# Kernel tuning notes

Measured on AMD Instinct MI355X. Metric: run time of the kernel, lower is better.

Reference implementation:

```python
import jax, jax.numpy as jnp
import numpy as np

N_FFT = 512
HOP = N_FFT // 4  # torch.stft default hop_length
SR = 16000
SS = 340.4
DIST = 1.0


def _hann(n):
    # torch.hann_window default is periodic
    return (0.5 * (1.0 - jnp.cos(2.0 * jnp.pi * jnp.arange(n) / n))).astype(jnp.float32)


def _stft(x):
    # x: [N, L] -> complex [N, F, T]; matches torch.stft(center=True, pad_mode='reflect', onesided=True)
    pad = N_FFT // 2
    xp = jnp.pad(x, ((0, 0), (pad, pad)), mode='reflect')
    T = (xp.shape[1] - N_FFT) // HOP + 1
    idx = jnp.arange(T)[:, None] * HOP + jnp.arange(N_FFT)[None, :]  # [T, n_fft]
    frames = xp[:, idx] * _hann(N_FFT)[None, None, :]                # [N, T, n_fft]
    X = jnp.fft.rfft(frames, axis=-1)                                # [N, T, F]
    return jnp.swapaxes(X, 1, 2)                                     # [N, F, T]


def setup_inputs() -> dict:
    key = jax.random.key(0)
    k1, k2, k3 = jax.random.split(key, 3)
    B, C, L = 16, 4, 160000
    x = jax.random.normal(k1, (B, C, L), dtype=jnp.float32)
    angle = jax.random.uniform(k2, (B, 1), dtype=jnp.float32) * 360.0
    mic_pos = jax.random.normal(k3, (B, C, 3), dtype=jnp.float32) * 0.05
    return {"x": x, "angle": angle, "mic_pos": mic_pos}


def reference(x, angle, mic_pos):
    B, C, L = x.shape
    X = _stft(x.reshape(B * C, L))            # [B*C, F, T] complex
    Fdim, T = X.shape[1], X.shape[2]
    X = X.reshape(B, C, Fdim, T)

    # 'X' feature: real/imag concat over channel dim -> [B, 2C, F, T]
    featX = jnp.concatenate([X.real, X.imag], axis=1)

    # 'SV' feature: steering vectors
    ang = angle[:, 0]
    half_pi = jnp.float32(np.pi / 2)
    sin90 = jnp.sin(half_pi)
    cos90 = jnp.cos(half_pi)  # ~0, kept for faithfulness
    rad = -ang * (jnp.pi / 180.0)
    loc_src = jnp.stack([
        DIST * jnp.cos(rad) * sin90,
        DIST * jnp.sin(rad) * sin90,
        jnp.full_like(ang, DIST * cos90),
    ], axis=1)  # [B, 3]

    # Original computes torch.norm over the FULL [B,3] difference per mic i (a scalar),
    # so TDOA is identical across batch: Frobenius norm over (B, 3) axes.
    TDOA = jnp.sqrt(jnp.sum((mic_pos - loc_src[:, None, :]) ** 2, axis=(0, 2)))  # [C]
    TDOA = TDOA - TDOA[0]
    TDOA = jnp.broadcast_to(TDOA[None, :], (B, C))  # [B, C]

    # Steering[b,c,f] = exp(f * TDOA[b,c] * const), const = -1j*2*pi*sr/(n_fft*ss)
    coef = -2.0 * jnp.pi * SR / (N_FFT * SS)
    phase = coef * jnp.arange(Fdim, dtype=jnp.float32)[None, None, :] * TDOA[:, :, None]  # [B,C,F]
    sv = jnp.exp(1j * phase)  # complex64, unit magnitude
    sv = sv / jnp.linalg.norm(sv, axis=1, keepdims=True)  # normalize over channels
    sv = jnp.broadcast_to(sv[..., None], (B, C, Fdim, T))
    featSV = jnp.concatenate([sv.real, sv.imag], axis=1)  # [B, 2C, F, T]

    feature = jnp.concatenate([featX, featSV], axis=1)    # [B, 4C, F, T]
    feature = feature.reshape(B, 4 * C * Fdim, T)
    return jnp.transpose(feature, (0, 2, 1))               # [B, T, 4C*F]
```

## Files before the change

kernel.cpp:

```cpp
#include <hip/hip_runtime.h>
#include <math.h>

#define L_SIG 160000
#define HOPC 128
#define FD 257
#define TDIM 1251
#define ROW 4112
#define NROWS (16 * TDIM)

typedef float floatx4 __attribute__((ext_vector_type(4)));


__global__ __launch_bounds__(256) void setup_kernel(const float* __restrict__ angle,
                                                    const float* __restrict__ mic,
                                                    float* __restrict__ tbl) {
    int tid = threadIdx.x;
    __shared__ float tdoa[4];
    if (tid == 0) {
        const float half_pi = (float)(M_PI / 2.0);
        float s90 = sinf(half_pi);
        float c90 = cosf(half_pi);
        float acc0 = 0.f, acc1 = 0.f, acc2 = 0.f, acc3 = 0.f;
        for (int b = 0; b < 16; ++b) {
            float ang = angle[b];
            float rad = -ang * (float)(M_PI / 180.0);
            float lx = cosf(rad) * s90;
            float ly = sinf(rad) * s90;
            float lz = c90;
            #pragma unroll
            for (int c = 0; c < 4; ++c) {
                const float* m = mic + ((size_t)b * 4 + c) * 3;
                float dx = m[0] - lx, dy = m[1] - ly, dz = m[2] - lz;
                float s = dx * dx + dy * dy + dz * dz;
                if (c == 0) acc0 += s; else if (c == 1) acc1 += s;
                else if (c == 2) acc2 += s; else acc3 += s;
            }
        }
        float t0 = sqrtf(acc0);
        tdoa[0] = 0.0f;
        tdoa[1] = sqrtf(acc1) - t0;
        tdoa[2] = sqrtf(acc2) - t0;
        tdoa[3] = sqrtf(acc3) - t0;
    }
    __syncthreads();
    const float coef = (float)(-2.0 * M_PI * 16000.0 / (512.0 * 340.4));
    for (int i = tid; i < 4 * FD; i += 256) {
        int c = i / FD;
        int f = i - c * FD;
        float ph = coef * (float)f * tdoa[c];
        tbl[i]        = cosf(ph) * 0.5f;
        tbl[1028 + i] = sinf(ph) * 0.5f;
    }
}

__device__ __forceinline__ void bfly8(float (&zr)[8], float (&zi)[8]) {
    const float C = 0.70710678118654752440f;
    float sr0=zr[0]+zr[4], si0=zi[0]+zi[4], dr0=zr[0]-zr[4], di0=zi[0]-zi[4];
    float sr1=zr[1]+zr[5], si1=zi[1]+zi[5], dr1=zr[1]-zr[5], di1=zi[1]-zi[5];
    float sr2=zr[2]+zr[6], si2=zi[2]+zi[6], dr2=zr[2]-zr[6], di2=zi[2]-zi[6];
    float sr3=zr[3]+zr[7], si3=zi[3]+zi[7], dr3=zr[3]-zr[7], di3=zi[3]-zi[7];
    float t;
    t = C*(dr1+di1); di1 = C*(di1-dr1); dr1 = t;
    t = dr2; dr2 = di2; di2 = -t;
    t = C*(di3-dr3); di3 = -C*(dr3+di3); dr3 = t;
    float p0r=sr0+sr2, p0i=si0+si2, p1r=sr1+sr3, p1i=si1+si3;
    float q0r=sr0-sr2, q0i=si0-si2, q1r=sr1-sr3, q1i=si1-si3;
    zr[0]=p0r+p1r; zi[0]=p0i+p1i;
    zr[2]=q0r+q1i; zi[2]=q0i-q1r;
    zr[4]=p0r-p1r; zi[4]=p0i-p1i;
    zr[6]=q0r-q1i; zi[6]=q0i+q1r;
    p0r=dr0+dr2; p0i=di0+di2; p1r=dr1+dr3; p1i=di1+di3;
    q0r=dr0-dr2; q0i=di0-di2; q1r=dr1-dr3; q1i=di1-di3;
    zr[1]=p0r+p1r; zi[1]=p0i+p1i;
    zr[3]=q0r+q1i; zi[3]=q0i-q1r;
    zr[5]=p0r-p1r; zi[5]=p0i-p1i;
    zr[7]=q0r-q1i; zi[7]=q0i+q1r;
}

__device__ __forceinline__ void cmul(float& r, float& i, float ar, float ai, float br, float bi) {
    r = ar * br - ai * bi;
    i = ar * bi + ai * br;
}

__device__ __forceinline__ void twiddle8(float (&zr)[8], float (&zi)[8], float wr, float wi) {
    float p2r, p2i, p3r, p3i, p4r, p4i, p5r, p5i, p6r, p6i, p7r, p7i;
    cmul(p2r, p2i, wr, wi, wr, wi);
    cmul(p3r, p3i, p2r, p2i, wr, wi);
    cmul(p4r, p4i, p2r, p2i, p2r, p2i);
    cmul(p5r, p5i, p4r, p4i, wr, wi);
    cmul(p6r, p6i, p3r, p3i, p3r, p3i);
    cmul(p7r, p7i, p4r, p4i, p3r, p3i);
    float t;
    t = zr[1]*wr - zi[1]*wi;  zi[1] = zr[1]*wi + zi[1]*wr;  zr[1] = t;
    t = zr[2]*p2r - zi[2]*p2i; zi[2] = zr[2]*p2i + zi[2]*p2r; zr[2] = t;
    t = zr[3]*p3r - zi[3]*p3i; zi[3] = zr[3]*p3i + zi[3]*p3r; zr[3] = t;
    t = zr[4]*p4r - zi[4]*p4i; zi[4] = zr[4]*p4i + zi[4]*p4r; zr[4] = t;
    t = zr[5]*p5r - zi[5]*p5i; zi[5] = zr[5]*p5i + zi[5]*p5r; zr[5] = t;
    t = zr[6]*p6r - zi[6]*p6i; zi[6] = zr[6]*p6i + zi[6]*p6r; zr[6] = t;
    t = zr[7]*p7r - zi[7]*p7i; zi[7] = zr[7]*p7i + zi[7]*p7r; zr[7] = t;
}

#define PHYS(i) ((i) + ((i) >> 3))

__device__ __forceinline__ void fft512_pair(const float* __restrict__ xs0,
                                            const float* __restrict__ xs1,
                                            const int (&a)[8], const float (&w8)[8],
                                            float cj, float sj, float c1v, float s1v,
                                            int j, float2* buf,
                                            float (&F0r)[5], float (&F0i)[5],
                                            float (&F1r)[5], float (&F1i)[5]) {
    float zr[8], zi[8];
    #pragma unroll
    for (int r = 0; r < 8; ++r) {
        zr[r] = xs0[a[r]] * w8[r];
        zi[r] = xs1[a[r]] * w8[r];
    }

    bfly8(zr, zi);
    twiddle8(zr, zi, cj, -sj);
    #pragma unroll
    for (int k = 0; k < 8; ++k) buf[PHYS(8 * j + k)] = make_float2(zr[k], zi[k]);
    #pragma unroll
    for (int r = 0; r < 8; ++r) {
        float2 v = buf[PHYS(j + 64 * r)];
        zr[r] = v.x; zi[r] = v.y;
    }

    bfly8(zr, zi);
    twiddle8(zr, zi, c1v, -s1v);
    #pragma unroll
    for (int k = 0; k < 8; ++k) buf[PHYS(64 * (j >> 3) + (j & 7) + 8 * k)] = make_float2(zr[k], zi[k]);
    #pragma unroll
    for (int r = 0; r < 8; ++r) {
        float2 v = buf[PHYS(j + 64 * r)];
        zr[r] = v.x; zi[r] = v.y;
    }

    bfly8(zr, zi);

    const int srcl = (64 - j) & 63;
    float pr_[8], pi_[8];
    #pragma unroll
    for (int m = 0; m < 8; ++m) {
        pr_[m] = __shfl(zr[m], srcl, 64);
        pi_[m] = __shfl(zi[m], srcl, 64);
    }
    const bool l0 = (j == 0);
    #pragma unroll
    for (int k = 0; k < 5; ++k) {
        float Pr = l0 ? pr_[(8 - k) & 7] : pr_[7 - k];
        float Pi = l0 ? pi_[(8 - k) & 7] : pi_[7 - k];
        F0r[k] = 0.5f * (zr[k] + Pr);
        F0i[k] = 0.5f * (zi[k] - Pi);
        F1r[k] = 0.5f * (zi[k] + Pi);
        F1i[k] = 0.5f * (Pr - zr[k]);
    }
}

__global__ __launch_bounds__(256) void stft_row_kernel(const float* __restrict__ x,
                                                       const float* __restrict__ tbl,
                                                       float* __restrict__ out) {
    __shared__ floatx4 stg4[4][516];
    const int tid = threadIdx.x;
    const int wv  = tid >> 6;
    const int j   = tid & 63;
    const int wid = blockIdx.x * 4 + wv;
    const int b = wid / TDIM;
    const int t = wid - b * TDIM;

    const float PI_256 = 0.012271846303085129838f;
    float sj, cj;
    __sincosf((float)j * PI_256, &sj, &cj);
    const float R2 = 0.70710678118654752440f;
    float w8[8];
    w8[0] = 0.5f - 0.5f * cj;
    w8[1] = 0.5f - 0.5f * ((cj - sj) * R2);
    w8[2] = 0.5f + 0.5f * sj;
    w8[3] = 0.5f - 0.5f * ((-cj - sj) * R2);
    w8[4] = 0.5f + 0.5f * cj;
    w8[5] = 0.5f - 0.5f * ((sj - cj) * R2);
    w8[6] = 0.5f - 0.5f * sj;
    w8[7] = 0.5f - 0.5f * ((cj + sj) * R2);
    float s1v, c1v;
    __sincosf((float)(j & ~7) * PI_256, &s1v, &c1v);

    const int g = t * HOPC - 256 + j;
    int a[8];
    #pragma unroll
    for (int r = 0; r < 8; ++r) {
        int ar = g + 64 * r;
        ar = (ar < 0) ? -ar : ar;
        if (ar >= L_SIG) ar = 2 * L_SIG - 2 - ar;
        a[r] = ar;
    }

    float* stg  = (float*)&stg4[wv][0];
    float2* buf = (float2*)stg;

    const float* xb = x + (size_t)b * 4 * L_SIG;
    float A0r[5], A0i[5], A1r[5], A1i[5];
    float B0r[5], B0i[5], B1r[5], B1i[5];
    fft512_pair(xb,             xb + L_SIG,     a, w8, cj, sj, c1v, s1v, j, buf, A0r, A0i, A1r, A1i);
    fft512_pair(xb + 2 * L_SIG, xb + 3 * L_SIG, a, w8, cj, sj, c1v, s1v, j, buf, B0r, B0i, B1r, B1i);

    #pragma unroll
    for (int k = 0; k < 5; ++k) {
        int f = j + 64 * k;
        if (k < 4 || j == 0) {
            stg[f]        = A0r[k];
            stg[257 + f]  = A1r[k];
            stg[514 + f]  = B0r[k];
            stg[771 + f]  = B1r[k];
            stg[1028 + f] = A0i[k];
            stg[1285 + f] = A1i[k];
            stg[1542 + f] = B0i[k];
            stg[1799 + f] = B1i[k];
        }
    }

    const floatx4* sp = (const floatx4*)stg;
    floatx4* dst = (floatx4*)(out + (size_t)wid * ROW);
    #pragma unroll
    for (int it = 0; it < 8; ++it) {
        int i4 = 64 * it + j;
        __builtin_nontemporal_store(sp[i4], dst + i4);
    }
    if (j < 2) __builtin_nontemporal_store(sp[512 + j], dst + 512 + j);

    const floatx4* T4 = (const floatx4*)tbl;
    #pragma unroll
    for (int it = 0; it < 8; ++it) {
        int i4 = 64 * it + j;
        __builtin_nontemporal_store(T4[i4], dst + 514 + i4);
    }
    if (j < 2) __builtin_nontemporal_store(T4[512 + j], dst + 514 + 512 + j);
}

extern "C" void kernel_launch(void* const* d_in, const int* in_sizes, int n_in,
                              void* d_out, int out_size, void* d_ws, size_t ws_size,
                              hipStream_t stream) {
    const float* x     = (const float*)d_in[0];
    const float* angle = (const float*)d_in[1];
    const float* mic   = (const float*)d_in[2];
    float* out = (float*)d_out;
    float* tbl = (float*)d_ws;

    setup_kernel<<<1, 256, 0, stream>>>(angle, mic, tbl);
    stft_row_kernel<<<NROWS / 4, 256, 0, stream>>>(x, tbl, out);
}
```

Before: 367.7 us.

## Stage shared signal window in LDS per block of four overlapping frames

Each block now handles four consecutive frames of one batch item. It cooperatively loads the shared 896-sample window for all four channels into LDS with vectorized loads, falling back to scalar reflect-padded loads at the edges. The per-thread strided global loads with reflect index math are replaced by LDS reads, so the overlapping frames are no longer fetched again from global memory. The cost is a larger LDS footprint, two block-wide barriers, and a tail block with unused waves, since 1251 frames is not a multiple of 4.

```diff
diff --git a/kernel.cpp b/kernel.cpp
--- a/kernel.cpp
+++ b/kernel.cpp
@@ -7,6 +7,7 @@
 #define TDIM 1251
 #define ROW 4112
 #define NROWS (16 * TDIM)
+#define TBLK 313
 
 typedef float floatx4 __attribute__((ext_vector_type(4)));
 
@@ -102,20 +103,11 @@
 
 #define PHYS(i) ((i) + ((i) >> 3))
 
-__device__ __forceinline__ void fft512_pair(const float* __restrict__ xs0,
-                                            const float* __restrict__ xs1,
-                                            const int (&a)[8], const float (&w8)[8],
-                                            float cj, float sj, float c1v, float s1v,
-                                            int j, float2* buf,
-                                            float (&F0r)[5], float (&F0i)[5],
-                                            float (&F1r)[5], float (&F1i)[5]) {
-    float zr[8], zi[8];
-    #pragma unroll
-    for (int r = 0; r < 8; ++r) {
-        zr[r] = xs0[a[r]] * w8[r];
-        zi[r] = xs1[a[r]] * w8[r];
-    }
-
+__device__ __forceinline__ void fft_core(float (&zr)[8], float (&zi)[8],
+                                         float cj, float sj, float c1v, float s1v,
+                                         int j, float2* buf,
+                                         float (&F0r)[5], float (&F0i)[5],
+                                         float (&F1r)[5], float (&F1i)[5]) {
     bfly8(zr, zi);
     twiddle8(zr, zi, cj, -sj);
     #pragma unroll
@@ -157,16 +149,43 @@
     }
 }
 
-__global__ __launch_bounds__(256) void stft_row_kernel(const float* __restrict__ x,
-                                                       const float* __restrict__ tbl,
-                                                       float* __restrict__ out) {
-    __shared__ floatx4 stg4[4][516];
+__global__ __launch_bounds__(256, 4) void stft_row_kernel(const float* __restrict__ x,
+                                                          const float* __restrict__ tbl,
+                                                          float* __restrict__ out) {
+    __shared__ floatx4 ldsv[2056];
+    float* lds = (float*)ldsv;
     const int tid = threadIdx.x;
     const int wv  = tid >> 6;
     const int j   = tid & 63;
-    const int wid = blockIdx.x * 4 + wv;
-    const int b = wid / TDIM;
-    const int t = wid - b * TDIM;
+    const int b    = blockIdx.x / TBLK;
+    const int tblk = blockIdx.x - b * TBLK;
+    const int t0 = tblk * 4;
+    const int t  = t0 + wv;
+    const int g0 = t0 * HOPC - 256;
+
+    const float* xb = x + (size_t)b * 4 * L_SIG;
+    const bool interior = (g0 >= 0) && (g0 + 896 <= L_SIG);
+    if (interior) {
+        floatx4* d4 = (floatx4*)lds;
+        #pragma unroll
+        for (int it = 0; it < 4; ++it) {
+            int i = tid + 256 * it;
+            if (it < 3 || tid < 128) {
+                int c = i / 224, p = i - c * 224;
+                floatx4 v = *(const floatx4*)(xb + (size_t)c * L_SIG + g0 + 4 * p);
+                d4[i] = v;
+            }
+        }
+    } else {
+        for (int i = tid; i < 3584; i += 256) {
+            int c = i / 896, p = i - c * 896;
+            int gg = g0 + p;
+            gg = (gg < 0) ? -gg : gg;
+            if (gg >= L_SIG) gg = 2 * L_SIG - 2 - gg;
+            lds[c * 896 + p] = xb[(size_t)c * L_SIG + gg];
+        }
+    }
+    __syncthreads();
 
     const float PI_256 = 0.012271846303085129838f;
     float sj, cj;
@@ -184,56 +203,62 @@
     float s1v, c1v;
     __sincosf((float)(j & ~7) * PI_256, &s1v, &c1v);
 
-    const int g = t * HOPC - 256 + j;
-    int a[8];
-    #pragma unroll
-    for (int r = 0; r < 8; ++r) {
-        int ar = g + 64 * r;
-        ar = (ar < 0) ? -ar : ar;
-        if (ar >= L_SIG) ar = 2 * L_SIG - 2 - ar;
-        a[r] = ar;
-    }
-
-    float* stg  = (float*)&stg4[wv][0];
-    float2* buf = (float2*)stg;
-
-    const float* xb = x + (size_t)b * 4 * L_SIG;
+    float2* buf = (float2*)(lds + 3584) + wv * 576;
+    const int off = wv * HOPC + j;
+
     float A0r[5], A0i[5], A1r[5], A1i[5];
     float B0r[5], B0i[5], B1r[5], B1i[5];
-    fft512_pair(xb,             xb + L_SIG,     a, w8, cj, sj, c1v, s1v, j, buf, A0r, A0i, A1r, A1i);
-    fft512_pair(xb + 2 * L_SIG, xb + 3 * L_SIG, a, w8, cj, sj, c1v, s1v, j, buf, B0r, B0i, B1r, B1i);
-
-    #pragma unroll
-    for (int k = 0; k < 5; ++k) {
-        int f = j + 64 * k;
-        if (k < 4 || j == 0) {
-            stg[f]        = A0r[k];
-            stg[257 + f]  = A1r[k];
-            stg[514 + f]  = B0r[k];
-            stg[771 + f]  = B1r[k];
-            stg[1028 + f] = A0i[k];
-            stg[1285 + f] = A1i[k];
-            stg[1542 + f] = B0i[k];
-            stg[1799 + f] = B1i[k];
-        }
-    }
-
-    const floatx4* sp = (const floatx4*)stg;
-    floatx4* dst = (floatx4*)(out + (size_t)wid * ROW);
-    #pragma unroll
-    for (int it = 0; it < 8; ++it) {
-        int i4 = 64 * it + j;
-        __builtin_nontemporal_store(sp[i4], dst + i4);
-    }
-    if (j < 2) __builtin_nontemporal_store(sp[512 + j], dst + 512 + j);
-
-    const floatx4* T4 = (const floatx4*)tbl;
-    #pragma unroll
-    for (int it = 0; it < 8; ++it) {
-        int i4 = 64 * it + j;
-        __builtin_nontemporal_store(T4[i4], dst + 514 + i4);
-    }
-    if (j < 2) __builtin_nontemporal_store(T4[512 + j], dst + 514 + 512 + j);
+    float zr[8], zi[8];
+    #pragma unroll
+    for (int r = 0; r < 8; ++r) {
+        zr[r] = lds[off + 64 * r] * w8[r];
+        zi[r] = lds[896 + off + 64 * r] * w8[r];
+    }
+    fft_core(zr, zi, cj, sj, c1v, s1v, j, buf, A0r, A0i, A1r, A1i);
+    #pragma unroll
+    for (int r = 0; r < 8; ++r) {
+        zr[r] = lds[1792 + off + 64 * r] * w8[r];
+        zi[r] = lds[2688 + off + 64 * r] * w8[r];
+    }
+    fft_core(zr, zi, cj, sj, c1v, s1v, j, buf, B0r, B0i, B1r, B1i);
+
+    __syncthreads();
+
+    if (t < TDIM) {
+        float* stg = lds + wv * 2056;
+        #pragma unroll
+        for (int k = 0; k < 5; ++k) {
+            int f = j + 64 * k;
+            if (k < 4 || j == 0) {
+                stg[f]        = A0r[k];
+                stg[257 + f]  = A1r[k];
+                stg[514 + f]  = B0r[k];
+                stg[771 + f]  = B1r[k];
+                stg[1028 + f] = A0i[k];
+                stg[1285 + f] = A1i[k];
+                stg[1542 + f] = B0i[k];
+                stg[1799 + f] = B1i[k];
+            }
+        }
+
+        const int wid = b * TDIM + t;
+        const floatx4* sp = (const floatx4*)stg;
+        floatx4* dst = (floatx4*)(out + (size_t)wid * ROW);
+        #pragma unroll
+        for (int it = 0; it < 8; ++it) {
+            int i4 = 64 * it + j;
+            __builtin_nontemporal_store(sp[i4], dst + i4);
+        }
+        if (j < 2) __builtin_nontemporal_store(sp[512 + j], dst + 512 + j);
+
+        const floatx4* T4 = (const floatx4*)tbl;
+        #pragma unroll
+        for (int it = 0; it < 8; ++it) {
+            int i4 = 64 * it + j;
+            __builtin_nontemporal_store(T4[i4], dst + 514 + i4);
+        }
+        if (j < 2) __builtin_nontemporal_store(T4[512 + j], dst + 514 + 512 + j);
+    }
 }
 
 extern "C" void kernel_launch(void* const* d_in, const int* in_sizes, int n_in,
@@ -246,5 +271,5 @@
     float* tbl = (float*)d_ws;
 
     setup_kernel<<<1, 256, 0, stream>>>(angle, mic, tbl);
-    stft_row_kernel<<<NROWS / 4, 256, 0, stream>>>(x, tbl, out);
-}
+    stft_row_kernel<<<16 * TBLK, 256, 0, stream>>>(x, tbl, out);
+}
```

Measured after the change: 378.0 us. 2.8% more time.

## Shrink LDS staging to raise occupancy and issue table stores first

Applied to the files above, without the earlier changes.

The per-wave shared staging buffer is cut from 516 floatx4 to 576 float2 by writing the real and imaginary halves out in two passes that reuse the same buffer. The steering-vector table copy is moved to the start of the kernel so its stores overlap the FFT work, and launch bounds now request 6 blocks per CU. Together these aim to raise occupancy and hide memory latency in this store-bound kernel. The cost is an extra LDS write and read round, and possibly register pressure from the occupancy hint.

```diff
diff --git a/kernel.cpp b/kernel.cpp
--- a/kernel.cpp
+++ b/kernel.cpp
@@ -102,20 +102,11 @@
 
 #define PHYS(i) ((i) + ((i) >> 3))
 
-__device__ __forceinline__ void fft512_pair(const float* __restrict__ xs0,
-                                            const float* __restrict__ xs1,
-                                            const int (&a)[8], const float (&w8)[8],
-                                            float cj, float sj, float c1v, float s1v,
-                                            int j, float2* buf,
-                                            float (&F0r)[5], float (&F0i)[5],
-                                            float (&F1r)[5], float (&F1i)[5]) {
-    float zr[8], zi[8];
-    #pragma unroll
-    for (int r = 0; r < 8; ++r) {
-        zr[r] = xs0[a[r]] * w8[r];
-        zi[r] = xs1[a[r]] * w8[r];
-    }
-
+__device__ __forceinline__ void fft_core(float (&zr)[8], float (&zi)[8],
+                                         float cj, float sj, float c1v, float s1v,
+                                         int j, float2* buf,
+                                         float (&F0r)[5], float (&F0i)[5],
+                                         float (&F1r)[5], float (&F1i)[5]) {
     bfly8(zr, zi);
     twiddle8(zr, zi, cj, -sj);
     #pragma unroll
@@ -157,16 +148,26 @@
     }
 }
 
-__global__ __launch_bounds__(256) void stft_row_kernel(const float* __restrict__ x,
-                                                       const float* __restrict__ tbl,
-                                                       float* __restrict__ out) {
-    __shared__ floatx4 stg4[4][516];
+__global__ __launch_bounds__(256, 6) void stft_row_kernel(const float* __restrict__ x,
+                                                          const float* __restrict__ tbl,
+                                                          float* __restrict__ out) {
+    __shared__ float2 exch[4][576];
     const int tid = threadIdx.x;
     const int wv  = tid >> 6;
     const int j   = tid & 63;
     const int wid = blockIdx.x * 4 + wv;
     const int b = wid / TDIM;
     const int t = wid - b * TDIM;
+
+    floatx4* d4 = (floatx4*)(out + (size_t)wid * ROW);
+
+    const floatx4* T4 = (const floatx4*)tbl;
+    #pragma unroll
+    for (int it = 0; it < 8; ++it) {
+        int i4 = 64 * it + j;
+        __builtin_nontemporal_store(T4[i4], d4 + 514 + i4);
+    }
+    if (j < 2) __builtin_nontemporal_store(T4[512 + j], d4 + 514 + 512 + j);
 
     const float PI_256 = 0.012271846303085129838f;
     float sj, cj;
@@ -194,14 +195,25 @@
         a[r] = ar;
     }
 
-    float* stg  = (float*)&stg4[wv][0];
-    float2* buf = (float2*)stg;
-
+    float2* buf = exch[wv];
+    float* stg  = (float*)buf;
     const float* xb = x + (size_t)b * 4 * L_SIG;
+
     float A0r[5], A0i[5], A1r[5], A1i[5];
     float B0r[5], B0i[5], B1r[5], B1i[5];
-    fft512_pair(xb,             xb + L_SIG,     a, w8, cj, sj, c1v, s1v, j, buf, A0r, A0i, A1r, A1i);
-    fft512_pair(xb + 2 * L_SIG, xb + 3 * L_SIG, a, w8, cj, sj, c1v, s1v, j, buf, B0r, B0i, B1r, B1i);
+    float zr[8], zi[8];
+    #pragma unroll
+    for (int r = 0; r < 8; ++r) {
+        zr[r] = xb[a[r]] * w8[r];
+        zi[r] = xb[L_SIG + a[r]] * w8[r];
+    }
+    fft_core(zr, zi, cj, sj, c1v, s1v, j, buf, A0r, A0i, A1r, A1i);
+    #pragma unroll
+    for (int r = 0; r < 8; ++r) {
+        zr[r] = xb[2 * L_SIG + a[r]] * w8[r];
+        zi[r] = xb[3 * L_SIG + a[r]] * w8[r];
+    }
+    fft_core(zr, zi, cj, sj, c1v, s1v, j, buf, B0r, B0i, B1r, B1i);
 
     #pragma unroll
     for (int k = 0; k < 5; ++k) {
@@ -211,29 +223,37 @@
             stg[257 + f]  = A1r[k];
             stg[514 + f]  = B0r[k];
             stg[771 + f]  = B1r[k];
-            stg[1028 + f] = A0i[k];
-            stg[1285 + f] = A1i[k];
-            stg[1542 + f] = B0i[k];
-            stg[1799 + f] = B1i[k];
-        }
-    }
-
-    const floatx4* sp = (const floatx4*)stg;
-    floatx4* dst = (floatx4*)(out + (size_t)wid * ROW);
-    #pragma unroll
-    for (int it = 0; it < 8; ++it) {
-        int i4 = 64 * it + j;
-        __builtin_nontemporal_store(sp[i4], dst + i4);
-    }
-    if (j < 2) __builtin_nontemporal_store(sp[512 + j], dst + 512 + j);
-
-    const floatx4* T4 = (const floatx4*)tbl;
-    #pragma unroll
-    for (int it = 0; it < 8; ++it) {
-        int i4 = 64 * it + j;
-        __builtin_nontemporal_store(T4[i4], dst + 514 + i4);
-    }
-    if (j < 2) __builtin_nontemporal_store(T4[512 + j], dst + 514 + 512 + j);
+        }
+    }
+    {
+        const floatx4* sp = (const floatx4*)stg;
+        #pragma unroll
+        for (int it = 0; it < 4; ++it) {
+            int i4 = 64 * it + j;
+            __builtin_nontemporal_store(sp[i4], d4 + i4);
+        }
+        if (j == 0) __builtin_nontemporal_store(sp[256], d4 + 256);
+    }
+
+    #pragma unroll
+    for (int k = 0; k < 5; ++k) {
+        int f = j + 64 * k;
+        if (k < 4 || j == 0) {
+            stg[f]        = A0i[k];
+            stg[257 + f]  = A1i[k];
+            stg[514 + f]  = B0i[k];
+            stg[771 + f]  = B1i[k];
+        }
+    }
+    {
+        const floatx4* sp = (const floatx4*)stg;
+        #pragma unroll
+        for (int it = 0; it < 4; ++it) {
+            int i4 = 64 * it + j;
+            __builtin_nontemporal_store(sp[i4], d4 + 257 + i4);
+        }
+        if (j == 0) __builtin_nontemporal_store(sp[256], d4 + 257 + 256);
+    }
 }
 
 extern "C" void kernel_launch(void* const* d_in, const int* in_sizes, int n_in,
```

After: 400.7 us. 1.09x slower.
